# Optimization experiments

Hardware: AMD Instinct MI355X
Metric: run time of the kernel (lower is better)

The kernel has to match this reference:

```python
import jax, jax.numpy as jnp
import numpy as np

HP = 16          # hyber_para / embedding dim
NQ = 4           # qubits per subsystem (= log2(HP), also conv1 out channels)
NQ_AB = 8        # total circuit qubits
DIM_AB = 256     # 2**NQ_AB
W_MUL = (2.0 ** 0.5) * (5.0 ** -0.5)   # he_std with gain=sqrt(2), use_wscale=True, lrmul=1
VOCAB_D = 10000
VOCAB_T = 10000
LD = 262144
LT = 524288


def _np_kron_list(ms):
    out = ms[0]
    for m in ms[1:]:
        out = np.kron(out, m)
    return out


def _cnot_ring():
    # CNOT(0,1) ... CNOT(6,7) then CNOT(7,0); parameter-free, precompute in numpy.
    I = np.eye(2)
    X = np.array([[0.0, 1.0], [1.0, 0.0]])
    P0 = np.diag([1.0, 0.0])
    P1 = np.diag([0.0, 1.0])

    def cnot(c, t):
        f0 = [I] * NQ_AB; f0[c] = P0
        f1 = [I] * NQ_AB; f1[c] = P1; f1[t] = X
        return _np_kron_list(f0) + _np_kron_list(f1)

    U = np.eye(DIM_AB)
    for q in range(NQ_AB - 1):
        U = cnot(q, q + 1) @ U
    U = cnot(NQ_AB - 1, 0) @ U
    return U


CNOT_RING = jnp.asarray(_cnot_ring(), dtype=jnp.complex64)
# Pauli-Z sign patterns for per-qubit measurement (qubit 0 = most significant bit)
SIGNS = jnp.asarray(
    np.array([[1.0 - 2.0 * ((k >> (NQ - 1 - i)) & 1) for k in range(HP)] for i in range(NQ)]),
    dtype=jnp.float32)


def _rot(tx, ty, tz):
    # Rz(tz) @ Ry(ty) @ Rx(tx): rx applied first in the circuit
    hx, hy, hz = tx * 0.5, ty * 0.5, tz * 0.5
    cx, sx = jnp.cos(hx), jnp.sin(hx)
    cy, sy = jnp.cos(hy), jnp.sin(hy)
    zero = jnp.zeros((), jnp.complex64)
    Rx = jnp.array([[cx + 0j, -1j * sx], [-1j * sx, cx + 0j]], dtype=jnp.complex64)
    Ry = jnp.array([[cy + 0j, -sy + 0j], [sy + 0j, cy + 0j]], dtype=jnp.complex64)
    Rz = jnp.array([[jnp.exp(-1j * hz), zero], [zero, jnp.exp(1j * hz)]], dtype=jnp.complex64)
    return Rz @ Ry @ Rx


def _multi_kron(ms):
    out = ms[0]
    for m in ms[1:]:
        out = jnp.kron(out, m)
    return out


def _circuit_unitary(w):
    # Qu_mutual.qumutual(): rot layer -> cnot ring -> rot layer, 6 angles per qubit
    w = (w * W_MUL).reshape(NQ_AB, 6)
    L1 = _multi_kron([_rot(w[q, 0], w[q, 1], w[q, 2]) for q in range(NQ_AB)])
    L2 = _multi_kron([_rot(w[q, 3], w[q, 4], w[q, 5]) for q in range(NQ_AB)])
    return L2 @ CNOT_RING @ L1


def _encoding(x):
    # deepquantum encoding: density matrix (x @ dag(x)) / trace
    m = x @ x.T  # x real -> dag == transpose
    return (m / jnp.trace(m)).astype(jnp.complex64)


def _ptrace_first(rho):
    # trace out the first NQ-qubit subsystem of a (HP*HP)x(HP*HP) density matrix
    return jnp.einsum('ijik->jk', rho.reshape(HP, HP, HP, HP))


def _measure(rho):
    # per-qubit Pauli-Z expectations of a HPxHP density matrix -> (NQ, 1) real
    return (SIGNS @ jnp.real(jnp.diagonal(rho))).reshape(NQ, 1)


def _conv1d_same(x, w, b):
    # torch Conv1d padding='same', k=4 -> pad (left=1, right=2)
    y = jax.lax.conv_general_dilated(x, w, (1,), [(1, 2)],
                                     dimension_numbers=('NCH', 'OIH', 'NCH'))
    return y + b[None, :, None]


def _conv2d_p1(x, w, b):
    y = jax.lax.conv_general_dilated(x, w, (1, 1), [(1, 1), (1, 1)],
                                     dimension_numbers=('NCHW', 'OIHW', 'NCHW'))
    return y + b[None, :, None, None]


def _branch(idx, emb_w, w1, b1):
    emb = emb_w.at[0].set(0.0)                 # padding_idx=0
    e = emb[idx]                               # (L, HP)
    gram = e.T @ e                             # (HP, HP)
    c = _conv1d_same(gram.reshape(1, HP, HP), w1, b1).reshape(NQ, HP)  # (4, 16)
    return _encoding(c.T @ c), c @ c.T         # density (HP,HP) complex, pre-conv2 (NQ,NQ)


def _forward(drug, target, embed_drug_w, embed_target_w, dconv1_w, dconv1_b,
             tconv1_w, tconv1_b, dconv2_w, dconv2_b, tconv2_w, tconv2_b,
             mutual_w, fc1_w, fc1_b, fc2_w, fc2_b):
    d_rho, d_pre = _branch(drug, embed_drug_w, dconv1_w, dconv1_b)
    t_rho, t_pre = _branch(target, embed_target_w, tconv1_w, tconv1_b)
    U = _circuit_unitary(mutual_w)
    Ud = U.conj().T
    t1atd1 = _ptrace_first(U @ jnp.kron(d_rho, t_rho) @ Ud)   # (HP, HP)
    d1att1 = _ptrace_first(U @ jnp.kron(t_rho, d_rho) @ Ud)
    d_m = _measure(t1atd1)                                    # (NQ, 1)
    t_m = _measure(d1att1)
    d2 = _conv2d_p1(jnp.stack([d_pre, d_m @ d_m.T])[None], dconv2_w, dconv2_b)  # (1,4,4,4)
    t2 = _conv2d_p1(jnp.stack([t_pre, t_m @ t_m.T])[None], tconv2_w, tconv2_b)
    x = jnp.concatenate([d2, t2], axis=0).reshape(1, 2 * 4 * NQ * NQ)           # (1, 128)
    h = jax.nn.leaky_relu(x @ fc1_w.T + fc1_b)
    return jax.nn.leaky_relu(h @ fc2_w.T + fc2_b).reshape(1)


def setup_inputs() -> dict:
    key = jax.random.key(0)
    ks = jax.random.split(key, 12)
    return {
        'drug': jax.random.randint(ks[0], (LD,), 0, VOCAB_D),
        'target': jax.random.randint(ks[1], (LT,), 0, VOCAB_T),
        'embed_drug_w': jax.random.normal(ks[2], (VOCAB_D, HP), jnp.float32) * 0.05,
        'embed_target_w': jax.random.normal(ks[3], (VOCAB_T, HP), jnp.float32) * 0.05,
        'dconv1_w': jax.random.normal(ks[4], (NQ, HP, 4), jnp.float32) * 2e-4,
        'dconv1_b': jnp.zeros((NQ,), jnp.float32),
        'tconv1_w': jax.random.normal(ks[5], (NQ, HP, 4), jnp.float32) * 2e-4,
        'tconv1_b': jnp.zeros((NQ,), jnp.float32),
        'dconv2_w': jax.random.normal(ks[6], (4, 2, 3, 3), jnp.float32) * 0.1,
        'dconv2_b': jnp.zeros((4,), jnp.float32),
        'tconv2_w': jax.random.normal(ks[7], (4, 2, 3, 3), jnp.float32) * 0.1,
        'tconv2_b': jnp.zeros((4,), jnp.float32),
        'mutual_w': jax.random.uniform(ks[8], (6 * NQ_AB,), jnp.float32, 0.0, 2.0 * float(np.pi)),
        'fc1_w': jax.random.normal(ks[9], (32, 128), jnp.float32) * 0.05,
        'fc1_b': jnp.zeros((32,), jnp.float32),
        'fc2_w': jax.random.normal(ks[10], (1, 32), jnp.float32) * 0.05,
        'fc2_b': jnp.zeros((1,), jnp.float32),
    }


def reference(drug, target, embed_drug_w, embed_target_w, dconv1_w, dconv1_b,
              tconv1_w, tconv1_b, dconv2_w, dconv2_b, tconv2_w, tconv2_b,
              mutual_w, fc1_w, fc1_b, fc2_w, fc2_b):
    return _forward(drug, target, embed_drug_w, embed_target_w, dconv1_w, dconv1_b,
                    tconv1_w, tconv1_b, dconv2_w, dconv2_b, tconv2_w, tconv2_b,
                    mutual_w, fc1_w, fc1_b, fc2_w, fc2_b)
```

## Files before the change

kernel.cpp:

```cpp
#include <hip/hip_runtime.h>

#define VOC 10000

__device__ __forceinline__ float2 cmul(float2 a, float2 b) {
  return make_float2(a.x * b.x - a.y * b.y, a.x * b.y + a.y * b.x);
}
__device__ __forceinline__ float2 cmulj(float2 a, float2 b) {
  return make_float2(a.x * b.x + a.y * b.y, a.y * b.x - a.x * b.y);
}
__device__ __forceinline__ float2 cadd(float2 a, float2 b) {
  return make_float2(a.x + b.x, a.y + b.y);
}

__global__ __launch_bounds__(256) void hist_kernel(
    const int* __restrict__ drug, const int* __restrict__ target,
    int* __restrict__ part, float* __restrict__ gram_g,
    int* __restrict__ counter) {
  __shared__ int h[VOC];
  const int t = threadIdx.x, b = blockIdx.x;
  for (int i = t; i < VOC; i += 256) h[i] = 0;
  if (b == 0) {
    gram_g[t] = 0.f;
    gram_g[t + 256] = 0.f;
    if (t == 0) *counter = 0;
  }
  __syncthreads();
  const int* __restrict__ src = (b < 64) ? (drug + b * 4096)
                                         : (target + (b - 64) * 4096);
  const int4* __restrict__ s4 = (const int4*)src;
#pragma unroll
  for (int i = 0; i < 4; ++i) {
    int4 v = s4[i * 256 + t];
    atomicAdd(&h[v.x], 1);
    atomicAdd(&h[v.y], 1);
    atomicAdd(&h[v.z], 1);
    atomicAdd(&h[v.w], 1);
  }
  __syncthreads();
  int4* __restrict__ dst = (int4*)(part + b * VOC);
  const int4* __restrict__ hs = (const int4*)h;
  for (int i = t; i < VOC / 4; i += 256) dst[i] = hs[i];
}

__global__ __launch_bounds__(256) void gram_tail_kernel(
    const float* __restrict__ Ed, const float* __restrict__ Et,
    const int* __restrict__ part, float* __restrict__ gram_g,
    int* __restrict__ counter,
    const float* __restrict__ dw1, const float* __restrict__ db1,
    const float* __restrict__ tw1, const float* __restrict__ tb1,
    const float* __restrict__ dw2, const float* __restrict__ db2,
    const float* __restrict__ tw2, const float* __restrict__ tb2,
    const float* __restrict__ mw,
    const float* __restrict__ f1w, const float* __restrict__ f1b,
    const float* __restrict__ f2w, const float* __restrict__ f2b,
    float* __restrict__ out) {

  __shared__ float se[157 * 16];
  __shared__ float scnt[157];
  __shared__ int islast;
  __shared__ float wconv[2][256];
  __shared__ float sw2[2][72];
  __shared__ float sb1[2][4], sb2[2][4];
  __shared__ float smw[48];
  __shared__ float sf1b[32], sf2w[32], sf2b[1];
  __shared__ float sgram[512];
  __shared__ float cmat[2][4][16];
  __shared__ float Hmat[2][16];
  __shared__ float ssum[2];
  __shared__ float2 rotm[2][8][4];
  __shared__ float2 M16[4][256];
  __shared__ int gtab[2][16];
  __shared__ int ftab[2][16];
  __shared__ float2 pab[2][2][16][4];
  __shared__ float2 Ahs[2][4][16][4];
  __shared__ float2 Bhs[2][4][16][4];
  __shared__ float2 Qa[2][16][16];
  __shared__ float2 Qb[2][16][16];
  __shared__ float2 SQa[2][16];
  __shared__ float2 SQb[2][4][16];
  __shared__ float dmv[2][4];
  __shared__ float xv[128];
  __shared__ float hv[32];

  const int t = threadIdx.x, b = blockIdx.x;
  const float W_MUL = 0.6324555320336759f;

  const float4* f1w4 = (const float4*)f1w;
  float4 rw0 = f1w4[(t << 2) + 0];
  float4 rw1 = f1w4[(t << 2) + 1];
  float4 rw2 = f1w4[(t << 2) + 2];
  float4 rw3 = f1w4[(t << 2) + 3];
  wconv[0][t] = dw1[t];
  wconv[1][t] = tw1[t];
  if (t < 72) { sw2[0][t] = dw2[t]; sw2[1][t] = tw2[t]; }
  else if (t < 80) {
    const int br = (t - 72) >> 2, i = t & 3;
    sb1[br][i] = br ? tb1[i] : db1[i];
    sb2[br][i] = br ? tb2[i] : db2[i];
  } else if (t >= 128 && t < 176) smw[t - 128] = mw[t - 128];
  else if (t >= 192 && t < 224) sf2w[t - 192] = f2w[t - 192];
  else if (t >= 224) sf1b[t - 224] = f1b[t - 224];
  if (t == 100) sf2b[0] = f2b[0];

  const int br = b >> 6, local = b & 63;
  const int start = local * 157;
  const int n = (VOC - start < 157) ? (VOC - start) : 157;
  {
    const float* __restrict__ E = br ? Et : Ed;
    const float4* __restrict__ E4 = (const float4*)(E + start * 16);
    for (int e = t; e < n * 4; e += 256) ((float4*)se)[e] = E4[e];
    if (t < n) {
      const int v = start + t;
      const int* __restrict__ P = part + (br ? 64 * VOC : 0) + v;
      const int NP = br ? 128 : 64;
      int c = 0;
#pragma unroll 8
      for (int bb = 0; bb < NP; ++bb) c += P[bb * VOC];
      scnt[t] = (v == 0) ? 0.f : (float)c;
    }
  }
  __syncthreads();
  {
    const int a = t >> 4, col = t & 15;
    float acc = 0.f;
    for (int r = 0; r < n; ++r)
      acc = fmaf(scnt[r] * se[(r << 4) + a], se[(r << 4) + col], acc);
    atomicAdd(&gram_g[(br << 8) + t], acc);
  }

  if (t == 0) {
    __threadfence();
    islast = (atomicAdd(counter, 1) == 127);
  }
  __syncthreads();
  if (!islast) return;
  __threadfence();

  sgram[t] = __hip_atomic_load(&gram_g[t], __ATOMIC_RELAXED,
                               __HIP_MEMORY_SCOPE_AGENT);
  sgram[t + 256] = __hip_atomic_load(&gram_g[t + 256], __ATOMIC_RELAXED,
                                     __HIP_MEMORY_SCOPE_AGENT);
  __syncthreads();

  if (t < 128) {
    const int brx = t >> 6, o = (t >> 4) & 3, p = t & 15;
    float s = sb1[brx][o];
    const float* g = &sgram[brx << 8];
    const float* w = wconv[brx];
    for (int i = 0; i < 16; ++i) {
#pragma unroll
      for (int k = 0; k < 4; ++k) {
        int q = p + k - 1;
        if (q >= 0 && q < 16) s = fmaf(w[(o << 6) + (i << 2) + k], g[(i << 4) + q], s);
      }
    }
    cmat[brx][o][p] = s;
  } else if (t < 144) {
    const int idx = t - 128, l = idx >> 3, q = idx & 7;
    float hx = 0.5f * W_MUL * smw[q * 6 + l * 3 + 0];
    float hy = 0.5f * W_MUL * smw[q * 6 + l * 3 + 1];
    float hz = 0.5f * W_MUL * smw[q * 6 + l * 3 + 2];
    float cx = cosf(hx), sx = sinf(hx);
    float cy = cosf(hy), sy = sinf(hy);
    float cz = cosf(hz), sz = sinf(hz);
    float2 m00 = make_float2(cy * cx, sy * sx);
    float2 m01 = make_float2(-sy * cx, -cy * sx);
    float2 m10 = make_float2(sy * cx, -cy * sx);
    float2 m11 = make_float2(cy * cx, -sy * sx);
    float2 e0 = make_float2(cz, -sz), e1 = make_float2(cz, sz);
    rotm[l][q][0] = cmul(e0, m00);
    rotm[l][q][1] = cmul(e0, m01);
    rotm[l][q][2] = cmul(e1, m10);
    rotm[l][q][3] = cmul(e1, m11);
  } else if (t < 208) {
    const int idx = t - 144;
    const int which = idx >> 5, par = (idx >> 4) & 1, nib = idx & 15;
    int b0 = (nib >> 3) & 1, b1 = (nib >> 2) & 1, b2 = (nib >> 1) & 1, b3 = nib & 1;
    if (which == 0) {
      int p0 = b1 ^ b2 ^ b3 ^ par;
      int p1 = b0 ^ b1, p2 = p1 ^ b2, p3 = p2 ^ b3;
      gtab[par][nib] = (p0 << 3) | (p1 << 2) | (p2 << 1) | p3;
    } else {
      int p4 = par ^ b0, p5 = p4 ^ b1, p6 = p5 ^ b2, p7 = p6 ^ b3;
      ftab[par][nib] = (p4 << 3) | (p5 << 2) | (p6 << 1) | p7;
    }
  }
  __syncthreads();

  if (t < 32) {
    const int brx = t >> 4, a = (t >> 2) & 3, bb = t & 3;
    float s = 0.f;
#pragma unroll
    for (int p = 0; p < 16; ++p) s = fmaf(cmat[brx][a][p], cmat[brx][bb][p], s);
    Hmat[brx][(a << 2) + bb] = s;
  }
#pragma unroll
  for (int mat = 0; mat < 4; ++mat) {
    const int r = t >> 4, c = t & 15;
    const int l = mat >> 1, qb = (mat & 1) << 2;
    float2 prod = rotm[l][qb + 0][(((r >> 3) & 1) << 1) | ((c >> 3) & 1)];
    prod = cmul(prod, rotm[l][qb + 1][(((r >> 2) & 1) << 1) | ((c >> 2) & 1)]);
    prod = cmul(prod, rotm[l][qb + 2][(((r >> 1) & 1) << 1) | ((c >> 1) & 1)]);
    prod = cmul(prod, rotm[l][qb + 3][((r & 1) << 1) | (c & 1)]);
    M16[mat][t] = prod;
  }
  __syncthreads();

  if (t < 2) {
    float s = 0.f;
#pragma unroll
    for (int i = 0; i < 16; ++i) s = fmaf(Hmat[t][i], Hmat[t][i], s);
    ssum[t] = s;
  }
  {
    const int op = t >> 7, brx = (t >> 6) & 1, r = (t >> 2) & 15, ca = t & 3;
    float2 s = make_float2(0.f, 0.f);
#pragma unroll
    for (int k = 0; k < 16; ++k) {
      float gk = cmat[brx][ca][k];
      float2 m = M16[op][(r << 4) + k];
      s.x = fmaf(m.x, gk, s.x);
      s.y = fmaf(m.y, gk, s.y);
    }
    pab[op][brx][r][ca] = s;
  }
  __syncthreads();

#pragma unroll
  for (int e0 = 0; e0 < 4; ++e0) {
    const int e = t + (e0 << 8);
    const int isB = e >> 9, rest = e & 511;
    const int ord = rest >> 8, s = (rest >> 6) & 3, row = (rest >> 2) & 15, cc = rest & 3;
    const int delta = s >> 1, eps = s & 1;
    float2 acc = make_float2(0.f, 0.f);
    if (!isB) {
      const int br1 = ord;
      for (int jh = 0; jh < 16; ++jh) {
        if ((__popc(jh) & 1) != delta) continue;
        acc = cadd(acc, cmul(M16[2][(row << 4) + gtab[eps][jh]], pab[0][br1][jh][cc]));
      }
      Ahs[ord][s][row][cc] = acc;
    } else {
      const int br2 = ord ^ 1;
      for (int jl = 0; jl < 16; ++jl) {
        if ((__popc(jl) & 1) != eps) continue;
        acc = cadd(acc, cmul(M16[3][(row << 4) + ftab[delta][jl]], pab[1][br2][jl][cc]));
      }
      Bhs[ord][s][row][cc] = acc;
    }
  }
  __syncthreads();

#pragma unroll
  for (int e0 = 0; e0 < 4; ++e0) {
    const int e = t + (e0 << 8);
    const int isb = e >> 9, rest = e & 511;
    const int ord = rest >> 8, ss = (rest >> 4) & 15, row = rest & 15;
    const int s = ss >> 2, sp = ss & 3;
    float2 u[4], w[4];
    const float* Hx;
    if (!isb) {
      Hx = Hmat[ord];
#pragma unroll
      for (int k = 0; k < 4; ++k) { u[k] = Ahs[ord][s][row][k]; w[k] = Ahs[ord][sp][row][k]; }
    } else {
      Hx = Hmat[ord ^ 1];
#pragma unroll
      for (int k = 0; k < 4; ++k) { u[k] = Bhs[ord][s][row][k]; w[k] = Bhs[ord][sp][row][k]; }
    }
    float2 acc = make_float2(0.f, 0.f);
#pragma unroll
    for (int a = 0; a < 4; ++a)
#pragma unroll
      for (int bb = 0; bb < 4; ++bb) {
        float2 v = cmulj(u[a], w[bb]);
        float hh = Hx[(a << 2) + bb];
        acc.x = fmaf(hh, v.x, acc.x);
        acc.y = fmaf(hh, v.y, acc.y);
      }
    if (!isb) Qa[ord][ss][row] = acc;
    else      Qb[ord][ss][row] = acc;
  }
  __syncthreads();

  if (t < 32) {
    const int ord = t >> 4, ss = t & 15;
    float2 acc = make_float2(0.f, 0.f);
#pragma unroll
    for (int r = 0; r < 16; ++r) acc = cadd(acc, Qa[ord][ss][r]);
    SQa[ord][ss] = acc;
  } else if (t >= 128) {
    const int idx = t - 128;
    const int ord = idx >> 6, i = (idx >> 4) & 3, ss = idx & 15;
    float2 acc = make_float2(0.f, 0.f);
#pragma unroll
    for (int ml = 0; ml < 16; ++ml) {
      float sg = ((ml >> (3 - i)) & 1) ? -1.f : 1.f;
      float2 q = Qb[ord][ss][ml];
      acc.x = fmaf(sg, q.x, acc.x);
      acc.y = fmaf(sg, q.y, acc.y);
    }
    SQb[ord][i][ss] = acc;
  }
  __syncthreads();

  if (t < 8) {
    const int ord = t >> 2, i = t & 3;
    float acc = 0.f;
#pragma unroll
    for (int ss = 0; ss < 16; ++ss) {
      float2 a = SQa[ord][ss], bq = SQb[ord][i][ss];
      acc += a.x * bq.x - a.y * bq.y;
    }
    dmv[ord][i] = acc / (ssum[0] * ssum[1]);
  }
  __syncthreads();

  if (t < 128) {
    const int brx = t >> 6, idx = t & 63;
    const int o = idx >> 4, yy = (idx >> 2) & 3, xx = idx & 3;
    float s = sb2[brx][o];
    for (int ch = 0; ch < 2; ++ch)
      for (int ky = 0; ky < 3; ++ky)
        for (int kx = 0; kx < 3; ++kx) {
          int iy = yy + ky - 1, ix = xx + kx - 1;
          if (iy < 0 || iy > 3 || ix < 0 || ix > 3) continue;
          float inv = (ch == 0) ? Hmat[brx][(iy << 2) + ix] : dmv[brx][iy] * dmv[brx][ix];
          s = fmaf(sw2[brx][o * 18 + ch * 9 + ky * 3 + kx], inv, s);
        }
    xv[(brx << 6) + idx] = s;
  }
  __syncthreads();

  {
    const int o = t >> 3, p = t & 7;
    const float* xp = &xv[p << 4];
    float s = 0.f;
    s = fmaf(rw0.x, xp[0], s);  s = fmaf(rw0.y, xp[1], s);
    s = fmaf(rw0.z, xp[2], s);  s = fmaf(rw0.w, xp[3], s);
    s = fmaf(rw1.x, xp[4], s);  s = fmaf(rw1.y, xp[5], s);
    s = fmaf(rw1.z, xp[6], s);  s = fmaf(rw1.w, xp[7], s);
    s = fmaf(rw2.x, xp[8], s);  s = fmaf(rw2.y, xp[9], s);
    s = fmaf(rw2.z, xp[10], s); s = fmaf(rw2.w, xp[11], s);
    s = fmaf(rw3.x, xp[12], s); s = fmaf(rw3.y, xp[13], s);
    s = fmaf(rw3.z, xp[14], s); s = fmaf(rw3.w, xp[15], s);
    s += __shfl_xor(s, 1);
    s += __shfl_xor(s, 2);
    s += __shfl_xor(s, 4);
    if (p == 0) {
      float v = s + sf1b[o];
      hv[o] = v > 0.f ? v : 0.01f * v;
    }
  }
  __syncthreads();

  if (t == 0) {
    float s = sf2b[0];
#pragma unroll
    for (int k = 0; k < 32; ++k) s = fmaf(hv[k], sf2w[k], s);
    s = s > 0.f ? s : 0.01f * s;
    out[0] = s;
  }
}

extern "C" void kernel_launch(void* const* d_in, const int* in_sizes, int n_in,
                              void* d_out, int out_size, void* d_ws, size_t ws_size,
                              hipStream_t stream) {
  const int* drug = (const int*)d_in[0];
  const int* target = (const int*)d_in[1];
  const float* embd = (const float*)d_in[2];
  const float* embt = (const float*)d_in[3];
  const float* dw1 = (const float*)d_in[4];
  const float* db1 = (const float*)d_in[5];
  const float* tw1 = (const float*)d_in[6];
  const float* tb1 = (const float*)d_in[7];
  const float* dw2 = (const float*)d_in[8];
  const float* db2 = (const float*)d_in[9];
  const float* tw2 = (const float*)d_in[10];
  const float* tb2 = (const float*)d_in[11];
  const float* mw = (const float*)d_in[12];
  const float* f1w = (const float*)d_in[13];
  const float* f1b = (const float*)d_in[14];
  const float* f2w = (const float*)d_in[15];
  const float* f2b = (const float*)d_in[16];

  int* part = (int*)d_ws;
  float* gram_g = (float*)(part + 192 * VOC);
  int* counter = (int*)(gram_g + 512);

  hist_kernel<<<dim3(192), dim3(256), 0, stream>>>(drug, target, part,
                                                   gram_g, counter);
  gram_tail_kernel<<<dim3(128), dim3(256), 0, stream>>>(
      embd, embt, part, gram_g, counter,
      dw1, db1, tw1, tb1, dw2, db2, tw2, tb2, mw,
      f1w, f1b, f2w, f2b, (float*)d_out);
}
```

Measured before the change: 31.81 us.

## Fuse histogram and gram kernels with grid barrier and 16-bit packed partial counts

Merges the histogram kernel and the gram/tail kernel into one 192-block launch that synchronises through a spin-wait grid barrier on a global counter. Partial histograms are packed as two 16-bit counts per word, halving the partial-count traffic. The gram work is spread over 192 blocks, and the parameter setup (rotation matrices, tables) overlaps with the counting phase. It adds a memset launch and relies on all 192 blocks being co-resident for the barrier to avoid deadlock.

```diff
diff --git a/kernel.cpp b/kernel.cpp
--- a/kernel.cpp
+++ b/kernel.cpp
@@ -1,6 +1,7 @@
 #include <hip/hip_runtime.h>
 
 #define VOC 10000
+#define NBLK 192
 
 __device__ __forceinline__ float2 cmul(float2 a, float2 b) {
   return make_float2(a.x * b.x - a.y * b.y, a.x * b.y + a.y * b.x);
@@ -12,40 +13,9 @@
   return make_float2(a.x + b.x, a.y + b.y);
 }
 
-__global__ __launch_bounds__(256) void hist_kernel(
+__global__ __launch_bounds__(256, 1) void fused_kernel(
     const int* __restrict__ drug, const int* __restrict__ target,
-    int* __restrict__ part, float* __restrict__ gram_g,
-    int* __restrict__ counter) {
-  __shared__ int h[VOC];
-  const int t = threadIdx.x, b = blockIdx.x;
-  for (int i = t; i < VOC; i += 256) h[i] = 0;
-  if (b == 0) {
-    gram_g[t] = 0.f;
-    gram_g[t + 256] = 0.f;
-    if (t == 0) *counter = 0;
-  }
-  __syncthreads();
-  const int* __restrict__ src = (b < 64) ? (drug + b * 4096)
-                                         : (target + (b - 64) * 4096);
-  const int4* __restrict__ s4 = (const int4*)src;
-#pragma unroll
-  for (int i = 0; i < 4; ++i) {
-    int4 v = s4[i * 256 + t];
-    atomicAdd(&h[v.x], 1);
-    atomicAdd(&h[v.y], 1);
-    atomicAdd(&h[v.z], 1);
-    atomicAdd(&h[v.w], 1);
-  }
-  __syncthreads();
-  int4* __restrict__ dst = (int4*)(part + b * VOC);
-  const int4* __restrict__ hs = (const int4*)h;
-  for (int i = t; i < VOC / 4; i += 256) dst[i] = hs[i];
-}
-
-__global__ __launch_bounds__(256) void gram_tail_kernel(
     const float* __restrict__ Ed, const float* __restrict__ Et,
-    const int* __restrict__ part, float* __restrict__ gram_g,
-    int* __restrict__ counter,
     const float* __restrict__ dw1, const float* __restrict__ db1,
     const float* __restrict__ tw1, const float* __restrict__ tb1,
     const float* __restrict__ dw2, const float* __restrict__ db2,
@@ -53,10 +23,11 @@
     const float* __restrict__ mw,
     const float* __restrict__ f1w, const float* __restrict__ f1b,
     const float* __restrict__ f2w, const float* __restrict__ f2b,
-    float* __restrict__ out) {
-
-  __shared__ float se[157 * 16];
-  __shared__ float scnt[157];
+    float* __restrict__ out, int* __restrict__ ws) {
+
+  __shared__ int h[VOC];
+  __shared__ float se[106 * 16];
+  __shared__ float scnt[106];
   __shared__ int islast;
   __shared__ float wconv[2][256];
   __shared__ float sw2[2][72];
@@ -85,6 +56,11 @@
   const int t = threadIdx.x, b = blockIdx.x;
   const float W_MUL = 0.6324555320336759f;
 
+  int* c0 = ws;
+  int* c1 = ws + 1;
+  float* gram_g = (float*)(ws + 4);
+  unsigned* part16 = (unsigned*)(ws + 516);
+
   const float4* f1w4 = (const float4*)f1w;
   float4 rw0 = f1w4[(t << 2) + 0];
   float4 rw1 = f1w4[(t << 2) + 1];
@@ -102,61 +78,64 @@
   else if (t >= 224) sf1b[t - 224] = f1b[t - 224];
   if (t == 100) sf2b[0] = f2b[0];
 
-  const int br = b >> 6, local = b & 63;
-  const int start = local * 157;
-  const int n = (VOC - start < 157) ? (VOC - start) : 157;
+  for (int i = t; i < VOC; i += 256) h[i] = 0;
+  __syncthreads();
   {
+    const int* __restrict__ src = (b < 64) ? (drug + (b << 12))
+                                           : (target + ((b - 64) << 12));
+    const int4* __restrict__ s4 = (const int4*)src;
+#pragma unroll
+    for (int i = 0; i < 4; ++i) {
+      int4 v = s4[i * 256 + t];
+      atomicAdd(&h[v.x], 1);
+      atomicAdd(&h[v.y], 1);
+      atomicAdd(&h[v.z], 1);
+      atomicAdd(&h[v.w], 1);
+    }
+  }
+  __syncthreads();
+  {
+    unsigned* __restrict__ dst = part16 + b * 5000;
+    for (int i = t; i < 5000; i += 256) {
+      unsigned w = ((unsigned)h[2 * i] & 0xffffu) | ((unsigned)h[2 * i + 1] << 16);
+      __hip_atomic_store(&dst[i], w, __ATOMIC_RELAXED, __HIP_MEMORY_SCOPE_AGENT);
+    }
+  }
+
+  __threadfence();
+  __syncthreads();
+  if (t == 0) {
+    atomicAdd(c0, 1);
+    while (__hip_atomic_load(c0, __ATOMIC_ACQUIRE, __HIP_MEMORY_SCOPE_AGENT) < NBLK)
+      __builtin_amdgcn_s_sleep(2);
+  }
+  __syncthreads();
+
+  const int br = (b >= 96) ? 1 : 0;
+  const int start = (br ? (b - 96) : b) * 106;
+  const int n = (start < VOC) ? ((VOC - start < 106) ? (VOC - start) : 106) : 0;
+  if (n > 0) {
     const float* __restrict__ E = br ? Et : Ed;
     const float4* __restrict__ E4 = (const float4*)(E + start * 16);
     for (int e = t; e < n * 4; e += 256) ((float4*)se)[e] = E4[e];
-    if (t < n) {
-      const int v = start + t;
-      const int* __restrict__ P = part + (br ? 64 * VOC : 0) + v;
-      const int NP = br ? 128 : 64;
-      int c = 0;
-#pragma unroll 8
-      for (int bb = 0; bb < NP; ++bb) c += P[bb * VOC];
-      scnt[t] = (v == 0) ? 0.f : (float)c;
-    }
-  }
-  __syncthreads();
-  {
-    const int a = t >> 4, col = t & 15;
-    float acc = 0.f;
-    for (int r = 0; r < n; ++r)
-      acc = fmaf(scnt[r] * se[(r << 4) + a], se[(r << 4) + col], acc);
-    atomicAdd(&gram_g[(br << 8) + t], acc);
-  }
-
-  if (t == 0) {
-    __threadfence();
-    islast = (atomicAdd(counter, 1) == 127);
-  }
-  __syncthreads();
-  if (!islast) return;
-  __threadfence();
-
-  sgram[t] = __hip_atomic_load(&gram_g[t], __ATOMIC_RELAXED,
-                               __HIP_MEMORY_SCOPE_AGENT);
-  sgram[t + 256] = __hip_atomic_load(&gram_g[t + 256], __ATOMIC_RELAXED,
-                                     __HIP_MEMORY_SCOPE_AGENT);
-  __syncthreads();
-
-  if (t < 128) {
-    const int brx = t >> 6, o = (t >> 4) & 3, p = t & 15;
-    float s = sb1[brx][o];
-    const float* g = &sgram[brx << 8];
-    const float* w = wconv[brx];
-    for (int i = 0; i < 16; ++i) {
-#pragma unroll
-      for (int k = 0; k < 4; ++k) {
-        int q = p + k - 1;
-        if (q >= 0 && q < 16) s = fmaf(w[(o << 6) + (i << 2) + k], g[(i << 4) + q], s);
+  }
+  if (t < 53) {
+    if (2 * t < n) {
+      const int gp = (start >> 1) + t;
+      const int blk0 = br ? 64 : 0, NP = br ? 128 : 64;
+      unsigned cA = 0, cB = 0;
+#pragma unroll 16
+      for (int bb = 0; bb < NP; ++bb) {
+        unsigned w = part16[(blk0 + bb) * 5000 + gp];
+        cA += w & 0xffffu;
+        cB += w >> 16;
       }
-    }
-    cmat[brx][o][p] = s;
-  } else if (t < 144) {
-    const int idx = t - 128, l = idx >> 3, q = idx & 7;
+      const int v0 = start + 2 * t;
+      scnt[2 * t] = (v0 == 0) ? 0.f : (float)cA;
+      scnt[2 * t + 1] = (float)cB;
+    }
+  } else if (t >= 64 && t < 80) {
+    const int idx = t - 64, l = idx >> 3, q = idx & 7;
     float hx = 0.5f * W_MUL * smw[q * 6 + l * 3 + 0];
     float hy = 0.5f * W_MUL * smw[q * 6 + l * 3 + 1];
     float hz = 0.5f * W_MUL * smw[q * 6 + l * 3 + 2];
@@ -172,8 +151,8 @@
     rotm[l][q][1] = cmul(e0, m01);
     rotm[l][q][2] = cmul(e1, m10);
     rotm[l][q][3] = cmul(e1, m11);
-  } else if (t < 208) {
-    const int idx = t - 144;
+  } else if (t >= 96 && t < 160) {
+    const int idx = t - 96;
     const int which = idx >> 5, par = (idx >> 4) & 1, nib = idx & 15;
     int b0 = (nib >> 3) & 1, b1 = (nib >> 2) & 1, b2 = (nib >> 1) & 1, b3 = nib & 1;
     if (which == 0) {
@@ -187,13 +166,6 @@
   }
   __syncthreads();
 
-  if (t < 32) {
-    const int brx = t >> 4, a = (t >> 2) & 3, bb = t & 3;
-    float s = 0.f;
-#pragma unroll
-    for (int p = 0; p < 16; ++p) s = fmaf(cmat[brx][a][p], cmat[brx][bb][p], s);
-    Hmat[brx][(a << 2) + bb] = s;
-  }
 #pragma unroll
   for (int mat = 0; mat < 4; ++mat) {
     const int r = t >> 4, c = t & 15;
@@ -204,13 +176,51 @@
     prod = cmul(prod, rotm[l][qb + 3][((r & 1) << 1) | (c & 1)]);
     M16[mat][t] = prod;
   }
-  __syncthreads();
-
-  if (t < 2) {
+
+  if (n > 0) {
+    const int a = t >> 4, col = t & 15;
+    float acc = 0.f;
+    for (int r = 0; r < n; ++r)
+      acc = fmaf(scnt[r] * se[(r << 4) + a], se[(r << 4) + col], acc);
+    atomicAdd(&gram_g[(br << 8) + t], acc);
+  }
+
+  if (t == 0) {
+    __threadfence();
+    islast = (atomicAdd(c1, 1) == NBLK - 1);
+  }
+  __syncthreads();
+  if (!islast) return;
+  __threadfence();
+
+  sgram[t] = __hip_atomic_load(&gram_g[t], __ATOMIC_RELAXED,
+                               __HIP_MEMORY_SCOPE_AGENT);
+  sgram[t + 256] = __hip_atomic_load(&gram_g[t + 256], __ATOMIC_RELAXED,
+                                     __HIP_MEMORY_SCOPE_AGENT);
+  __syncthreads();
+
+  if (t < 128) {
+    const int brx = t >> 6, o = (t >> 4) & 3, p = t & 15;
+    float s = sb1[brx][o];
+    const float* g = &sgram[brx << 8];
+    const float* w = wconv[brx];
+    for (int i = 0; i < 16; ++i) {
+#pragma unroll
+      for (int k = 0; k < 4; ++k) {
+        int q = p + k - 1;
+        if (q >= 0 && q < 16) s = fmaf(w[(o << 6) + (i << 2) + k], g[(i << 4) + q], s);
+      }
+    }
+    cmat[brx][o][p] = s;
+  }
+  __syncthreads();
+
+  if (t < 32) {
+    const int brx = t >> 4, a = (t >> 2) & 3, bb = t & 3;
     float s = 0.f;
 #pragma unroll
-    for (int i = 0; i < 16; ++i) s = fmaf(Hmat[t][i], Hmat[t][i], s);
-    ssum[t] = s;
+    for (int p = 0; p < 16; ++p) s = fmaf(cmat[brx][a][p], cmat[brx][bb][p], s);
+    Hmat[brx][(a << 2) + bb] = s;
   }
   {
     const int op = t >> 7, brx = (t >> 6) & 1, r = (t >> 2) & 15, ca = t & 3;
@@ -226,6 +236,12 @@
   }
   __syncthreads();
 
+  if (t < 2) {
+    float s = 0.f;
+#pragma unroll
+    for (int i = 0; i < 16; ++i) s = fmaf(Hmat[t][i], Hmat[t][i], s);
+    ssum[t] = s;
+  }
 #pragma unroll
   for (int e0 = 0; e0 < 4; ++e0) {
     const int e = t + (e0 << 8);
@@ -384,14 +400,9 @@
   const float* f2w = (const float*)d_in[15];
   const float* f2b = (const float*)d_in[16];
 
-  int* part = (int*)d_ws;
-  float* gram_g = (float*)(part + 192 * VOC);
-  int* counter = (int*)(gram_g + 512);
-
-  hist_kernel<<<dim3(192), dim3(256), 0, stream>>>(drug, target, part,
-                                                   gram_g, counter);
-  gram_tail_kernel<<<dim3(128), dim3(256), 0, stream>>>(
-      embd, embt, part, gram_g, counter,
+  hipMemsetAsync(d_ws, 0, 2064, stream);
+  fused_kernel<<<dim3(NBLK), dim3(256), 0, stream>>>(
+      drug, target, embd, embt,
       dw1, db1, tw1, tb1, dw2, db2, tw2, tb2, mw,
-      f1w, f1b, f2w, f2b, (float*)d_out);
+      f1w, f1b, f2w, f2b, (float*)d_out, (int*)d_ws);
 }
```

New measurement: 49.40 us. 1.55x slower.

## Pack partial histograms to 16-bit and hoist rotation setup before last-block barrier

Applied to the files above, without the earlier changes.

Each per-block partial histogram is now stored as packed 16-bit pairs, which halves the bytes written by the histogram kernel and read back during the count reduction. Each block holds 4096 tokens, so a count fits in 16 bits. The rotation matrices, parity tables and M16 products are now computed by every block alongside the count loading, before the last-block election, which takes them off the serial tail. The threadfence calls are replaced with an explicit s_waitcnt plus barrier, which relies on the atomic ordering that instruction gives.

```diff
diff --git a/kernel.cpp b/kernel.cpp
--- a/kernel.cpp
+++ b/kernel.cpp
@@ -12,9 +12,10 @@
   return make_float2(a.x + b.x, a.y + b.y);
 }
 
+
 __global__ __launch_bounds__(256) void hist_kernel(
     const int* __restrict__ drug, const int* __restrict__ target,
-    int* __restrict__ part, float* __restrict__ gram_g,
+    unsigned* __restrict__ part16, float* __restrict__ gram_g,
     int* __restrict__ counter) {
   __shared__ int h[VOC];
   const int t = threadIdx.x, b = blockIdx.x;
@@ -25,8 +26,8 @@
     if (t == 0) *counter = 0;
   }
   __syncthreads();
-  const int* __restrict__ src = (b < 64) ? (drug + b * 4096)
-                                         : (target + (b - 64) * 4096);
+  const int* __restrict__ src = (b < 64) ? (drug + (b << 12))
+                                         : (target + ((b - 64) << 12));
   const int4* __restrict__ s4 = (const int4*)src;
 #pragma unroll
   for (int i = 0; i < 4; ++i) {
@@ -37,14 +38,14 @@
     atomicAdd(&h[v.w], 1);
   }
   __syncthreads();
-  int4* __restrict__ dst = (int4*)(part + b * VOC);
-  const int4* __restrict__ hs = (const int4*)h;
-  for (int i = t; i < VOC / 4; i += 256) dst[i] = hs[i];
+  unsigned* __restrict__ dst = part16 + b * 5000;
+  for (int i = t; i < 5000; i += 256)
+    dst[i] = ((unsigned)h[2 * i] & 0xffffu) | ((unsigned)h[2 * i + 1] << 16);
 }
 
 __global__ __launch_bounds__(256) void gram_tail_kernel(
     const float* __restrict__ Ed, const float* __restrict__ Et,
-    const int* __restrict__ part, float* __restrict__ gram_g,
+    const unsigned* __restrict__ part16, float* __restrict__ gram_g,
     int* __restrict__ counter,
     const float* __restrict__ dw1, const float* __restrict__ db1,
     const float* __restrict__ tw1, const float* __restrict__ tb1,
@@ -109,54 +110,27 @@
     const float* __restrict__ E = br ? Et : Ed;
     const float4* __restrict__ E4 = (const float4*)(E + start * 16);
     for (int e = t; e < n * 4; e += 256) ((float4*)se)[e] = E4[e];
-    if (t < n) {
-      const int v = start + t;
-      const int* __restrict__ P = part + (br ? 64 * VOC : 0) + v;
-      const int NP = br ? 128 : 64;
-      int c = 0;
-#pragma unroll 8
-      for (int bb = 0; bb < NP; ++bb) c += P[bb * VOC];
-      scnt[t] = (v == 0) ? 0.f : (float)c;
-    }
-  }
-  __syncthreads();
-  {
-    const int a = t >> 4, col = t & 15;
-    float acc = 0.f;
-    for (int r = 0; r < n; ++r)
-      acc = fmaf(scnt[r] * se[(r << 4) + a], se[(r << 4) + col], acc);
-    atomicAdd(&gram_g[(br << 8) + t], acc);
-  }
-
-  if (t == 0) {
-    __threadfence();
-    islast = (atomicAdd(counter, 1) == 127);
-  }
-  __syncthreads();
-  if (!islast) return;
-  __threadfence();
-
-  sgram[t] = __hip_atomic_load(&gram_g[t], __ATOMIC_RELAXED,
-                               __HIP_MEMORY_SCOPE_AGENT);
-  sgram[t + 256] = __hip_atomic_load(&gram_g[t + 256], __ATOMIC_RELAXED,
-                                     __HIP_MEMORY_SCOPE_AGENT);
-  __syncthreads();
-
-  if (t < 128) {
-    const int brx = t >> 6, o = (t >> 4) & 3, p = t & 15;
-    float s = sb1[brx][o];
-    const float* g = &sgram[brx << 8];
-    const float* w = wconv[brx];
-    for (int i = 0; i < 16; ++i) {
-#pragma unroll
-      for (int k = 0; k < 4; ++k) {
-        int q = p + k - 1;
-        if (q >= 0 && q < 16) s = fmaf(w[(o << 6) + (i << 2) + k], g[(i << 4) + q], s);
-      }
-    }
-    cmat[brx][o][p] = s;
-  } else if (t < 144) {
-    const int idx = t - 128, l = idx >> 3, q = idx & 7;
+  }
+  __syncthreads();
+
+  const int wstart = start >> 1;
+  const int wn = (((start + n - 1) >> 1) - wstart) + 1;
+  if (t < wn) {
+    const int wg = wstart + t;
+    const unsigned* __restrict__ P = part16 + (br ? 64 * 5000 : 0) + wg;
+    const int NP = br ? 128 : 64;
+    unsigned cA = 0, cB = 0;
+#pragma unroll 16
+    for (int bb = 0; bb < NP; ++bb) {
+      unsigned w = P[bb * 5000];
+      cA += w & 0xffffu;
+      cB += w >> 16;
+    }
+    const int vA = wg << 1, vB = vA | 1;
+    if (vA >= start && vA < start + n) scnt[vA - start] = (vA == 0) ? 0.f : (float)cA;
+    if (vB >= start && vB < start + n) scnt[vB - start] = (float)cB;
+  } else if (t >= 96 && t < 112) {
+    const int idx = t - 96, l = idx >> 3, q = idx & 7;
     float hx = 0.5f * W_MUL * smw[q * 6 + l * 3 + 0];
     float hy = 0.5f * W_MUL * smw[q * 6 + l * 3 + 1];
     float hz = 0.5f * W_MUL * smw[q * 6 + l * 3 + 2];
@@ -172,8 +146,8 @@
     rotm[l][q][1] = cmul(e0, m01);
     rotm[l][q][2] = cmul(e1, m10);
     rotm[l][q][3] = cmul(e1, m11);
-  } else if (t < 208) {
-    const int idx = t - 144;
+  } else if (t >= 128 && t < 192) {
+    const int idx = t - 128;
     const int which = idx >> 5, par = (idx >> 4) & 1, nib = idx & 15;
     int b0 = (nib >> 3) & 1, b1 = (nib >> 2) & 1, b2 = (nib >> 1) & 1, b3 = nib & 1;
     if (which == 0) {
@@ -187,13 +161,6 @@
   }
   __syncthreads();
 
-  if (t < 32) {
-    const int brx = t >> 4, a = (t >> 2) & 3, bb = t & 3;
-    float s = 0.f;
-#pragma unroll
-    for (int p = 0; p < 16; ++p) s = fmaf(cmat[brx][a][p], cmat[brx][bb][p], s);
-    Hmat[brx][(a << 2) + bb] = s;
-  }
 #pragma unroll
   for (int mat = 0; mat < 4; ++mat) {
     const int r = t >> 4, c = t & 15;
@@ -204,13 +171,49 @@
     prod = cmul(prod, rotm[l][qb + 3][((r & 1) << 1) | (c & 1)]);
     M16[mat][t] = prod;
   }
-  __syncthreads();
-
-  if (t < 2) {
+
+  {
+    const int a = t >> 4, col = t & 15;
+    float acc = 0.f;
+    for (int r = 0; r < n; ++r)
+      acc = fmaf(scnt[r] * se[(r << 4) + a], se[(r << 4) + col], acc);
+    atomicAdd(&gram_g[(br << 8) + t], acc);
+  }
+
+  asm volatile("s_waitcnt vmcnt(0)" ::: "memory");
+  __syncthreads();
+  if (t == 0) islast = (atomicAdd(counter, 1) == 127);
+  __syncthreads();
+  if (!islast) return;
+
+  sgram[t] = __hip_atomic_load(&gram_g[t], __ATOMIC_RELAXED,
+                               __HIP_MEMORY_SCOPE_AGENT);
+  sgram[t + 256] = __hip_atomic_load(&gram_g[t + 256], __ATOMIC_RELAXED,
+                                     __HIP_MEMORY_SCOPE_AGENT);
+  __syncthreads();
+
+  if (t < 128) {
+    const int brx = t >> 6, o = (t >> 4) & 3, p = t & 15;
+    float s = sb1[brx][o];
+    const float* g = &sgram[brx << 8];
+    const float* w = wconv[brx];
+    for (int i = 0; i < 16; ++i) {
+#pragma unroll
+      for (int k = 0; k < 4; ++k) {
+        int q = p + k - 1;
+        if (q >= 0 && q < 16) s = fmaf(w[(o << 6) + (i << 2) + k], g[(i << 4) + q], s);
+      }
+    }
+    cmat[brx][o][p] = s;
+  }
+  __syncthreads();
+
+  if (t < 32) {
+    const int brx = t >> 4, a = (t >> 2) & 3, bb = t & 3;
     float s = 0.f;
 #pragma unroll
-    for (int i = 0; i < 16; ++i) s = fmaf(Hmat[t][i], Hmat[t][i], s);
-    ssum[t] = s;
+    for (int p = 0; p < 16; ++p) s = fmaf(cmat[brx][a][p], cmat[brx][bb][p], s);
+    Hmat[brx][(a << 2) + bb] = s;
   }
   {
     const int op = t >> 7, brx = (t >> 6) & 1, r = (t >> 2) & 15, ca = t & 3;
@@ -226,6 +229,12 @@
   }
   __syncthreads();
 
+  if (t < 2) {
+    float s = 0.f;
+#pragma unroll
+    for (int i = 0; i < 16; ++i) s = fmaf(Hmat[t][i], Hmat[t][i], s);
+    ssum[t] = s;
+  }
 #pragma unroll
   for (int e0 = 0; e0 < 4; ++e0) {
     const int e = t + (e0 << 8);
@@ -384,14 +393,15 @@
   const float* f2w = (const float*)d_in[15];
   const float* f2b = (const float*)d_in[16];
 
-  int* part = (int*)d_ws;
-  float* gram_g = (float*)(part + 192 * VOC);
-  int* counter = (int*)(gram_g + 512);
-
-  hist_kernel<<<dim3(192), dim3(256), 0, stream>>>(drug, target, part,
+  int* ws = (int*)d_ws;
+  int* counter = ws;
+  float* gram_g = (float*)(ws + 4);
+  unsigned* part16 = (unsigned*)(ws + 516);
+
+  hist_kernel<<<dim3(192), dim3(256), 0, stream>>>(drug, target, part16,
                                                    gram_g, counter);
   gram_tail_kernel<<<dim3(128), dim3(256), 0, stream>>>(
-      embd, embt, part, gram_g, counter,
+      embd, embt, part16, gram_g, counter,
       dw1, db1, tw1, tb1, dw2, db2, tw2, tb2, mw,
       f1w, f1b, f2w, f2b, (float*)d_out);
 }
```

Result: faster. 30.60 us (-3.8%).
